# Kernel optimization log

Measured on AMD Instinct MI355X. Metric: run time of the kernel, lower is better.

Reference implementation:

```python
import jax, jax.numpy as jnp
import numpy as np

B, M, N, D, H = 8, 64, 64, 256, 8

def setup_inputs() -> dict:
    key = jax.random.key(0)
    kx, kq, kk, kv, ko = jax.random.split(key, 5)
    x = jax.random.normal(kx, (B, M, N, D), dtype=jnp.float32)
    q = jax.random.normal(kq, (H, D, D), dtype=jnp.float32)
    k = jax.random.normal(kk, (D, D), dtype=jnp.float32)
    v = jax.random.normal(kv, (D, D), dtype=jnp.float32)
    o = jax.random.normal(ko, (H, D, D), dtype=jnp.float32)
    return {"x": x, "q": q, "k": k, "v": v, "o": o}

def reference(x, q, k, v, o):
    # x: [b,m,n,d]; q,o: [h,d,d]; k,v: [d,d]
    Q = jnp.einsum('bmnd,hdk->bhmnk', x, q)      # [b,h,m,n,d]
    h_half = Q.shape[1] // 2
    Q1, Q2 = Q[:, :h_half], Q[:, h_half:]
    K = jnp.einsum('bmnd,dk->bmnk', x, k)        # [b,m,n,d]
    V = jnp.einsum('bmnd,dv->bmnv', x, v)        # [b,m,n,d]

    # Axis 1: attend along the m (row) axis for each column y
    logits1 = jnp.einsum('bhxyk,bzyk->bhyxz', Q1, K)   # [b,h/2,n,m,m]
    scores1 = jax.nn.softmax(logits1, axis=-1)
    O1 = jnp.einsum('bhyxz,bzyv->bhxyv', scores1, V)   # [b,h/2,m,n,d]

    # Axis 2: attend along the n (column) axis for each row x
    logits2 = jnp.einsum('bhxyk,bxzk->bhxyz', Q2, K)   # [b,h/2,m,n,n]
    scores2 = jax.nn.softmax(logits2, axis=-1)
    O2 = jnp.einsum('bhxyz,bxzv->bhxyv', scores2, V)   # [b,h/2,m,n,d]

    O = jnp.concatenate([O1, O2], axis=1)              # [b,h,m,n,d]
    # Faithful to original: 'bhmnd,hdv->bmnd' keeps d, sums over h and v
    Z = jnp.einsum('bhmnd,hdv->bmnd', O, o)
    return Z
```

## Files before the change

### kernel.cpp

```cpp
#include <hip/hip_runtime.h>

typedef unsigned short u16;
typedef __attribute__((ext_vector_type(8))) short short8;
typedef __attribute__((ext_vector_type(4))) float f32x4;

__device__ __forceinline__ float bf2f(u16 u){ return __uint_as_float(((unsigned)u)<<16); }
__device__ __forceinline__ u16 f2bf(float f){
  unsigned u = __float_as_uint(f);
  unsigned r = u + 0x7fffu + ((u>>16)&1u);
  return (u16)(r>>16);
}

#define MFMA16(a,b,c) __builtin_amdgcn_mfma_f32_16x16x32_bf16(a,b,c,0,0,0)

static constexpr int XS_STR  = 264;
static constexpr int PS_STR  = 72;
static constexpr int WT_STR  = 72;
static constexpr int XHI_OFF = 0;
static constexpr int XLO_OFF = 16896;
static constexpr int GT_OFF  = 33792;
static constexpr int XVT_OFF = 50688;
static constexpr int PS_OFF  = 69120;
static constexpr int SMEM_BYTES = 73728*2;

static constexpr int MH_SMEM = 70656*2;


__global__ void ksplit_kernel(const float* __restrict__ k,
                              u16* __restrict__ khi, u16* __restrict__ klo){
  int e = blockIdx.x*256 + threadIdx.x;
  float f = k[e];
  u16 hi = f2bf(f);
  khi[e] = hi;
  klo[e] = f2bf(f - bf2f(hi));
}

__global__ __launch_bounds__(256,1) void mh_kernel(
    const float* __restrict__ q, const u16* __restrict__ khi,
    const u16* __restrict__ klo, u16* __restrict__ mhi, u16* __restrict__ mlo)
{
  extern __shared__ u16 sm[];
  u16* Qhi = sm;
  u16* Qlo = sm + 16896;
  u16* Chi = sm + 33792;
  u16* Clo = sm + 52224;

  const int tid = threadIdx.x;
  const int w = tid >> 6, lane = tid & 63;
  const int quad = lane >> 4, m16 = lane & 15;
  const int cw = w << 6, koq = quad << 3;
  const int h = blockIdx.x >> 2, dt = (blockIdx.x & 3) << 6;

  #pragma unroll
  for (int i=0;i<16;i++){
    int idx4 = i*256 + tid;
    int tr = idx4 >> 6, c4 = (idx4 & 63) << 2;
    const float4 xv = *(const float4*)(q + (((h<<8)+dt+tr)<<8) + c4);
    ushort4 hv, lv;
    hv.x=f2bf(xv.x); lv.x=f2bf(xv.x-bf2f(hv.x));
    hv.y=f2bf(xv.y); lv.y=f2bf(xv.y-bf2f(hv.y));
    hv.z=f2bf(xv.z); lv.z=f2bf(xv.z-bf2f(hv.z));
    hv.w=f2bf(xv.w); lv.w=f2bf(xv.w-bf2f(hv.w));
    *(ushort4*)&Qhi[tr*XS_STR + c4] = hv;
    *(ushort4*)&Qlo[tr*XS_STR + c4] = lv;
  }
  __syncthreads();

  const f32x4 zf = {0.f,0.f,0.f,0.f};
  f32x4 acc[4][4];
  #pragma unroll
  for (int r=0;r<4;r++)
    #pragma unroll
    for (int c=0;c<4;c++) acc[r][c] = zf;

  short8 Bh[2][4], Bl[2][4];
  #pragma unroll
  for (int c=0;c<4;c++){
    Bh[0][c] = *(const short8*)&khi[(cw + c*16 + m16)*256 + koq];
    Bl[0][c] = *(const short8*)&klo[(cw + c*16 + m16)*256 + koq];
  }
  #pragma unroll
  for (int kk=0;kk<8;kk++){
    const int cur = kk&1, nxt = cur^1;
    if (kk<7){
      const int ko2 = ((kk+1)<<5) + koq;
      #pragma unroll
      for (int c=0;c<4;c++){
        Bh[nxt][c] = *(const short8*)&khi[(cw + c*16 + m16)*256 + ko2];
        Bl[nxt][c] = *(const short8*)&klo[(cw + c*16 + m16)*256 + ko2];
      }
    }
    const int ko = (kk<<5) + koq;
    short8 Ah[4], Al[4];
    #pragma unroll
    for (int r=0;r<4;r++) Ah[r] = *(const short8*)&Qhi[(r*16+m16)*XS_STR + ko];
    #pragma unroll
    for (int r=0;r<4;r++) Al[r] = *(const short8*)&Qlo[(r*16+m16)*XS_STR + ko];
    #pragma unroll
    for (int r=0;r<4;r++)
      #pragma unroll
      for (int c=0;c<4;c++){
        acc[r][c] = MFMA16(Ah[r], Bh[cur][c], acc[r][c]);
        acc[r][c] = MFMA16(Ah[r], Bl[cur][c], acc[r][c]);
        acc[r][c] = MFMA16(Al[r], Bh[cur][c], acc[r][c]);
      }
  }

  #pragma unroll
  for (int r=0;r<4;r++)
    #pragma unroll
    for (int c=0;c<4;c++)
      #pragma unroll
      for (int g=0; g<4; g++){
        int drow = r*16 + quad*4 + g;
        int dp   = cw + c*16 + m16;
        float vv = acc[r][c][g];
        u16 hh = f2bf(vv);
        Chi[dp*WT_STR + drow] = hh;
        Clo[dp*WT_STR + drow] = f2bf(vv - bf2f(hh));
      }
  __syncthreads();

  #pragma unroll
  for (int p=0;p<8;p++){
    int ch = tid + (p<<8);
    int dp = ch >> 3, i8 = (ch & 7) << 3;
    *(int4*)&mhi[(((h<<8)+dp)<<8) + dt + i8] = *(const int4*)&Chi[dp*WT_STR + i8];
    *(int4*)&mlo[(((h<<8)+dp)<<8) + dt + i8] = *(const int4*)&Clo[dp*WT_STR + i8];
  }
}

__global__ void vt_kernel(const float* __restrict__ v, u16* __restrict__ vT){
  __shared__ float Ts[64*65];
  const int tid = threadIdx.x;
  const int bi = (blockIdx.x>>2)<<6, bj = (blockIdx.x&3)<<6;
  #pragma unroll
  for (int p=0;p<4;p++){
    int idx4 = tid + (p<<8);
    int i = idx4 >> 4, c4 = (idx4 & 15) << 2;
    const float4 f4 = *(const float4*)(v + ((bi+i)<<8) + bj + c4);
    Ts[i*65+c4] = f4.x; Ts[i*65+c4+1] = f4.y; Ts[i*65+c4+2] = f4.z; Ts[i*65+c4+3] = f4.w;
  }
  __syncthreads();
  #pragma unroll
  for (int p=0;p<2;p++){
    int ch = tid + (p<<8);
    int j = ch >> 3, i8 = (ch & 7) << 3;
    short8 t8;
    #pragma unroll
    for (int e=0;e<8;e++) t8[e] = (short)f2bf(Ts[(i8+e)*65 + j]);
    *(short8*)&vT[((bj+j)<<8) + bi + i8] = t8;
  }
}

__global__ void so_kernel(const float* __restrict__ o, float* __restrict__ so){
  int h = blockIdx.x;
  int w = threadIdx.x >> 6, l = threadIdx.x & 63;
  for (int i=0;i<64;i++){
    int row = w*64 + i;
    const float4 f4 = *(const float4*)(o + (((h<<8)+row)<<8) + (l<<2));
    float s = f4.x + f4.y + f4.z + f4.w;
    #pragma unroll
    for (int off=32; off>=1; off>>=1) s += __shfl_xor(s, off, 64);
    if (l==0) so[(h<<8)+row] = s;
  }
}

template<int BR>
__global__ __launch_bounds__(256,1) void attn_kernel(
    const float* __restrict__ x, const u16* __restrict__ mhiP,
    const u16* __restrict__ mloP, const u16* __restrict__ vT,
    const float* __restrict__ soP, float* __restrict__ out)
{
  extern __shared__ u16 sm[];
  u16* Xhi = sm + XHI_OFF;
  u16* Xlo = sm + XLO_OFF;
  u16* Gt  = sm + GT_OFF;
  u16* Xvt = sm + XVT_OFF;
  u16* Ps  = sm + PS_OFF;

  const int tid  = threadIdx.x;
  const int w    = tid >> 6, lane = tid & 63;
  const int quad = lane >> 4, m16 = lane & 15;
  const int b    = blockIdx.x >> 6, s = blockIdx.x & 63;
  const int cw   = w << 6;
  const int koq  = quad << 3;

  auto tok = [&](int t)->int {
    int m = (BR==0) ? t : s;
    int n = (BR==0) ? s : t;
    return (((b<<6) + m) << 14) + (n << 8);
  };

  #pragma unroll
  for (int i=0;i<16;i++){
    int idx4 = i*256 + tid;
    int tr = idx4 >> 6, c4 = (idx4 & 63) << 2;
    const float4 xv = *(const float4*)(x + tok(tr) + c4);
    ushort4 hv, lv;
    hv.x=f2bf(xv.x); lv.x=f2bf(xv.x-bf2f(hv.x));
    hv.y=f2bf(xv.y); lv.y=f2bf(xv.y-bf2f(hv.y));
    hv.z=f2bf(xv.z); lv.z=f2bf(xv.z-bf2f(hv.z));
    hv.w=f2bf(xv.w); lv.w=f2bf(xv.w-bf2f(hv.w));
    *(ushort4*)&Xhi[tr*XS_STR + c4] = hv;
    *(ushort4*)&Xlo[tr*XS_STR + c4] = lv;
  }
  __syncthreads();

  const f32x4 zf = {0.f,0.f,0.f,0.f};
  f32x4 acc[4][4];

  auto mm3 = [&](const u16* __restrict__ Whi, const u16* __restrict__ Wlo){
    #pragma unroll
    for (int r=0;r<4;r++)
      #pragma unroll
      for (int c=0;c<4;c++) acc[r][c] = zf;
    short8 Bh[2][4], Bl[2][4];
    #pragma unroll
    for (int c=0;c<4;c++){
      Bh[0][c] = *(const short8*)&Whi[(cw + c*16 + m16)*256 + koq];
      Bl[0][c] = *(const short8*)&Wlo[(cw + c*16 + m16)*256 + koq];
    }
    #pragma unroll
    for (int kk=0;kk<8;kk++){
      const int cur = kk&1, nxt = cur^1;
      if (kk<7){
        const int ko2 = ((kk+1)<<5) + koq;
        #pragma unroll
        for (int c=0;c<4;c++){
          Bh[nxt][c] = *(const short8*)&Whi[(cw + c*16 + m16)*256 + ko2];
          Bl[nxt][c] = *(const short8*)&Wlo[(cw + c*16 + m16)*256 + ko2];
        }
      }
      const int ko = (kk<<5) + koq;
      short8 Ah[4], Al[4];
      #pragma unroll
      for (int r=0;r<4;r++) Ah[r] = *(const short8*)&Xhi[(r*16+m16)*XS_STR + ko];
      #pragma unroll
      for (int r=0;r<4;r++) Al[r] = *(const short8*)&Xlo[(r*16+m16)*XS_STR + ko];
      #pragma unroll
      for (int r=0;r<4;r++)
        #pragma unroll
        for (int c=0;c<4;c++){
          acc[r][c] = MFMA16(Ah[r], Bh[cur][c], acc[r][c]);
          acc[r][c] = MFMA16(Ah[r], Bl[cur][c], acc[r][c]);
          acc[r][c] = MFMA16(Al[r], Bh[cur][c], acc[r][c]);
        }
    }
  };

  {
    #pragma unroll
    for (int r=0;r<4;r++)
      #pragma unroll
      for (int c=0;c<4;c++) acc[r][c] = zf;
    #pragma unroll
    for (int kk=0;kk<8;kk++){
      const int ko = (kk<<5) + koq;
      short8 A[4], Bf[4];
      #pragma unroll
      for (int r=0;r<4;r++) A[r]  = *(const short8*)&Xhi[(r*16+m16)*XS_STR + ko];
      #pragma unroll
      for (int c=0;c<4;c++) Bf[c] = *(const short8*)&vT[(cw + c*16 + m16)*256 + ko];
      #pragma unroll
      for (int r=0;r<4;r++)
        #pragma unroll
        for (int c=0;c<4;c++) acc[r][c] = MFMA16(A[r], Bf[c], acc[r][c]);
    }
    #pragma unroll
    for (int r=0;r<4;r++)
      #pragma unroll
      for (int c=0;c<4;c++)
        #pragma unroll
        for (int g=0; g<4; g++){
          int z  = r*16 + quad*4 + g;
          int vc = cw + c*16 + m16;
          Xvt[vc*WT_STR + z] = f2bf(acc[r][c][g]);
        }
  }

  f32x4 Z[4][4];
  #pragma unroll
  for (int r=0;r<4;r++)
    #pragma unroll
    for (int c=0;c<4;c++) Z[r][c] = zf;

  for (int h=0; h<4; h++){
    const int gh = BR*4 + h;

    mm3(mhiP + gh*65536, mloP + gh*65536);
    #pragma unroll
    for (int r=0;r<4;r++)
      #pragma unroll
      for (int c=0;c<4;c++)
        #pragma unroll
        for (int g=0; g<4; g++){
          int row = r*16 + quad*4 + g;
          int col = cw + c*16 + m16;
          Gt[row*XS_STR + col] = f2bf(acc[r][c][g]);
        }
    __syncthreads();

    f32x4 L[4];
    #pragma unroll
    for (int c=0;c<4;c++) L[c] = zf;
    #pragma unroll
    for (int kk=0;kk<8;kk++){
      const int ko = (kk<<5) + koq;
      short8 A = *(const short8*)&Gt[(w*16+m16)*XS_STR + ko];
      #pragma unroll
      for (int c=0;c<4;c++)
        L[c] = MFMA16(A, *(const short8*)&Xhi[(c*16+m16)*XS_STR + ko], L[c]);
      #pragma unroll
      for (int c=0;c<4;c++)
        L[c] = MFMA16(A, *(const short8*)&Xlo[(c*16+m16)*XS_STR + ko], L[c]);
    }
    __syncthreads();
    #pragma unroll
    for (int r=0;r<4;r++)
      #pragma unroll
      for (int c=0;c<4;c++)
        #pragma unroll
        for (int g=0; g<4; g++){
          int row = r*16 + quad*4 + g;
          int col = cw + c*16 + m16;
          float vv = acc[r][c][g];
          u16 hh = f2bf(vv);
          Gt[row*XS_STR + col] = f2bf(vv - bf2f(hh));
        }
    __syncthreads();

    #pragma unroll
    for (int kk=0;kk<8;kk++){
      const int ko = (kk<<5) + koq;
      short8 A = *(const short8*)&Gt[(w*16+m16)*XS_STR + ko];
      #pragma unroll
      for (int c=0;c<4;c++)
        L[c] = MFMA16(A, *(const short8*)&Xhi[(c*16+m16)*XS_STR + ko], L[c]);
    }

    #pragma unroll
    for (int g=0; g<4; g++){
      float mx = fmaxf(fmaxf(L[0][g],L[1][g]), fmaxf(L[2][g],L[3][g]));
      #pragma unroll
      for (int off=1; off<16; off<<=1) mx = fmaxf(mx, __shfl_xor(mx, off, 64));
      float sum = 0.f;
      #pragma unroll
      for (int c=0;c<4;c++){ float e = __expf(L[c][g]-mx); L[c][g] = e; sum += e; }
      #pragma unroll
      for (int off=1; off<16; off<<=1) sum += __shfl_xor(sum, off, 64);
      float inv = 1.f / sum;
      int row = w*16 + quad*4 + g;
      #pragma unroll
      for (int c=0;c<4;c++) Ps[row*PS_STR + c*16 + m16] = f2bf(L[c][g]*inv);
    }
    __syncthreads();

    #pragma unroll
    for (int r=0;r<4;r++)
      #pragma unroll
      for (int c=0;c<4;c++) acc[r][c] = zf;
    #pragma unroll
    for (int kk=0;kk<2;kk++){
      const int ko = (kk<<5) + koq;
      short8 A[4], Bf[4];
      #pragma unroll
      for (int r=0;r<4;r++) A[r]  = *(const short8*)&Ps[(r*16+m16)*PS_STR + ko];
      #pragma unroll
      for (int c=0;c<4;c++) Bf[c] = *(const short8*)&Xvt[(cw + c*16 + m16)*WT_STR + ko];
      #pragma unroll
      for (int r=0;r<4;r++)
        #pragma unroll
        for (int c=0;c<4;c++) acc[r][c] = MFMA16(A[r], Bf[c], acc[r][c]);
    }
    float sc[4];
    #pragma unroll
    for (int c=0;c<4;c++) sc[c] = soP[gh*256 + cw + c*16 + m16];
    #pragma unroll
    for (int r=0;r<4;r++)
      #pragma unroll
      for (int c=0;c<4;c++)
        #pragma unroll
        for (int g=0; g<4; g++) Z[r][c][g] += sc[c]*acc[r][c][g];
  }

  #pragma unroll
  for (int r=0;r<4;r++)
    #pragma unroll
    for (int c=0;c<4;c++)
      #pragma unroll
      for (int g=0; g<4; g++){
        int t   = r*16 + quad*4 + g;
        int col = cw + c*16 + m16;
        int off = tok(t) + col;
        float vv = Z[r][c][g];
        if (BR==1) vv += out[off];
        out[off] = vv;
      }
}

extern "C" void kernel_launch(void* const* d_in, const int* in_sizes, int n_in,
                              void* d_out, int out_size, void* d_ws, size_t ws_size,
                              hipStream_t stream) {
  const float* x = (const float*)d_in[0];
  const float* q = (const float*)d_in[1];
  const float* k = (const float*)d_in[2];
  const float* v = (const float*)d_in[3];
  const float* o = (const float*)d_in[4];
  u16* ws   = (u16*)d_ws;
  u16* mhi  = ws;
  u16* mlo  = ws + 524288;
  u16* scr  = ws + 1048576;
  u16* khi  = scr;
  u16* klo  = scr + 65536;
  u16* vT   = scr;
  float* soP = (float*)(scr + 65536);
  float* out = (float*)d_out;

  ksplit_kernel<<<256, 256, 0, stream>>>(k, khi, klo);
  (void)hipFuncSetAttribute(reinterpret_cast<const void*>(&mh_kernel),
                            hipFuncAttributeMaxDynamicSharedMemorySize, MH_SMEM);
  mh_kernel<<<32, 256, MH_SMEM, stream>>>(q, khi, klo, mhi, mlo);
  vt_kernel<<<16, 256, 0, stream>>>(v, vT);
  so_kernel<<<8, 256, 0, stream>>>(o, soP);

  (void)hipFuncSetAttribute(reinterpret_cast<const void*>(&attn_kernel<0>),
                            hipFuncAttributeMaxDynamicSharedMemorySize, SMEM_BYTES);
  (void)hipFuncSetAttribute(reinterpret_cast<const void*>(&attn_kernel<1>),
                            hipFuncAttributeMaxDynamicSharedMemorySize, SMEM_BYTES);
  attn_kernel<0><<<512, 256, SMEM_BYTES, stream>>>(x, mhi, mlo, vT, soP, out);
  attn_kernel<1><<<512, 256, SMEM_BYTES, stream>>>(x, mhi, mlo, vT, soP, out);
}
```

Measured before the change: 404.0 us.

## Merge attention branches into one launch with 512-thread blocks and atomics

The two per-branch attention launches become a single 1024-block grid, and output is accumulated with atomicAdd into a zeroed buffer. Blocks grow to 512 threads (8 waves), each wave covering half the columns. The softmax row is split across two waves and recombined through a small shared-memory max/sum exchange. The k-split, v-transpose and o-rowsum prep kernels are fused into one wider launch. The aim is more waves per CU for latency hiding, lower per-thread register pressure and fewer launches. The cost is float atomics, an extra memset and an extra block-level barrier per head.

Result: faster. 355.1 us (-12.1%).

```diff
diff --git a/kernel.cpp b/kernel.cpp
--- a/kernel.cpp
+++ b/kernel.cpp
@@ -21,18 +21,62 @@
 static constexpr int GT_OFF  = 33792;
 static constexpr int XVT_OFF = 50688;
 static constexpr int PS_OFF  = 69120;
-static constexpr int SMEM_BYTES = 73728*2;
+static constexpr int SMRE_OFF= 73728;
+static constexpr int SMEM_BYTES = (73728 + 512)*2;
 
 static constexpr int MH_SMEM = 70656*2;
 
 
-__global__ void ksplit_kernel(const float* __restrict__ k,
-                              u16* __restrict__ khi, u16* __restrict__ klo){
-  int e = blockIdx.x*256 + threadIdx.x;
-  float f = k[e];
-  u16 hi = f2bf(f);
-  khi[e] = hi;
-  klo[e] = f2bf(f - bf2f(hi));
+__global__ void prep_kernel(const float* __restrict__ k, const float* __restrict__ v,
+                            const float* __restrict__ o, u16* __restrict__ khi,
+                            u16* __restrict__ klo, u16* __restrict__ vT,
+                            float* __restrict__ soP){
+  __shared__ float Ts[64*65];
+  const int blk = blockIdx.x, tid = threadIdx.x;
+  if (blk < 64){
+    int base = blk*1024 + tid*4;
+    const float4 f4 = *(const float4*)(k + base);
+    ushort4 hv, lv;
+    hv.x=f2bf(f4.x); lv.x=f2bf(f4.x-bf2f(hv.x));
+    hv.y=f2bf(f4.y); lv.y=f2bf(f4.y-bf2f(hv.y));
+    hv.z=f2bf(f4.z); lv.z=f2bf(f4.z-bf2f(hv.z));
+    hv.w=f2bf(f4.w); lv.w=f2bf(f4.w-bf2f(hv.w));
+    *(ushort4*)&khi[base] = hv;
+    *(ushort4*)&klo[base] = lv;
+  } else if (blk < 80){
+    int t = blk - 64;
+    const int bi = (t>>2)<<6, bj = (t&3)<<6;
+    #pragma unroll
+    for (int p=0;p<4;p++){
+      int idx4 = tid + (p<<8);
+      int i = idx4 >> 4, c4 = (idx4 & 15) << 2;
+      const float4 f4 = *(const float4*)(v + ((bi+i)<<8) + bj + c4);
+      Ts[i*65+c4]=f4.x; Ts[i*65+c4+1]=f4.y; Ts[i*65+c4+2]=f4.z; Ts[i*65+c4+3]=f4.w;
+    }
+    __syncthreads();
+    #pragma unroll
+    for (int p=0;p<2;p++){
+      int ch = tid + (p<<8);
+      int j = ch >> 3, i8 = (ch & 7) << 3;
+      short8 t8;
+      #pragma unroll
+      for (int e=0;e<8;e++) t8[e] = (short)f2bf(Ts[(i8+e)*65 + j]);
+      *(short8*)&vT[((bj+j)<<8) + bi + i8] = t8;
+    }
+  } else {
+    int p = blk - 80;
+    int h = p >> 5, base = (p & 31) << 3;
+    int w = tid >> 6, l = tid & 63;
+    #pragma unroll
+    for (int i=0;i<2;i++){
+      int row = base + w*2 + i;
+      const float4 f4 = *(const float4*)(o + (((h<<8)+row)<<8) + (l<<2));
+      float s = f4.x + f4.y + f4.z + f4.w;
+      #pragma unroll
+      for (int off=32; off>=1; off>>=1) s += __shfl_xor(s, off, 64);
+      if (l==0) soP[(h<<8)+row] = s;
+    }
+  }
 }
 
 __global__ __launch_bounds__(256,1) void mh_kernel(
@@ -130,44 +174,7 @@
   }
 }
 
-__global__ void vt_kernel(const float* __restrict__ v, u16* __restrict__ vT){
-  __shared__ float Ts[64*65];
-  const int tid = threadIdx.x;
-  const int bi = (blockIdx.x>>2)<<6, bj = (blockIdx.x&3)<<6;
-  #pragma unroll
-  for (int p=0;p<4;p++){
-    int idx4 = tid + (p<<8);
-    int i = idx4 >> 4, c4 = (idx4 & 15) << 2;
-    const float4 f4 = *(const float4*)(v + ((bi+i)<<8) + bj + c4);
-    Ts[i*65+c4] = f4.x; Ts[i*65+c4+1] = f4.y; Ts[i*65+c4+2] = f4.z; Ts[i*65+c4+3] = f4.w;
-  }
-  __syncthreads();
-  #pragma unroll
-  for (int p=0;p<2;p++){
-    int ch = tid + (p<<8);
-    int j = ch >> 3, i8 = (ch & 7) << 3;
-    short8 t8;
-    #pragma unroll
-    for (int e=0;e<8;e++) t8[e] = (short)f2bf(Ts[(i8+e)*65 + j]);
-    *(short8*)&vT[((bj+j)<<8) + bi + i8] = t8;
-  }
-}
-
-__global__ void so_kernel(const float* __restrict__ o, float* __restrict__ so){
-  int h = blockIdx.x;
-  int w = threadIdx.x >> 6, l = threadIdx.x & 63;
-  for (int i=0;i<64;i++){
-    int row = w*64 + i;
-    const float4 f4 = *(const float4*)(o + (((h<<8)+row)<<8) + (l<<2));
-    float s = f4.x + f4.y + f4.z + f4.w;
-    #pragma unroll
-    for (int off=32; off>=1; off>>=1) s += __shfl_xor(s, off, 64);
-    if (l==0) so[(h<<8)+row] = s;
-  }
-}
-
-template<int BR>
-__global__ __launch_bounds__(256,1) void attn_kernel(
+__global__ __launch_bounds__(512,2) void attn_kernel(
     const float* __restrict__ x, const u16* __restrict__ mhiP,
     const u16* __restrict__ mloP, const u16* __restrict__ vT,
     const float* __restrict__ soP, float* __restrict__ out)
@@ -178,23 +185,28 @@
   u16* Gt  = sm + GT_OFF;
   u16* Xvt = sm + XVT_OFF;
   u16* Ps  = sm + PS_OFF;
+  float* SMf = (float*)(sm + SMRE_OFF);
 
   const int tid  = threadIdx.x;
   const int w    = tid >> 6, lane = tid & 63;
   const int quad = lane >> 4, m16 = lane & 15;
-  const int b    = blockIdx.x >> 6, s = blockIdx.x & 63;
-  const int cw   = w << 6;
+  const int br   = blockIdx.x >> 9;
+  const int idx  = blockIdx.x & 511;
+  const int b    = idx >> 6, s = idx & 63;
+  const int cw   = w << 5;
+  const int rs   = (w >> 1) << 4;
+  const int zh   = w & 1;
   const int koq  = quad << 3;
 
   auto tok = [&](int t)->int {
-    int m = (BR==0) ? t : s;
-    int n = (BR==0) ? s : t;
+    int m = br ? s : t;
+    int n = br ? t : s;
     return (((b<<6) + m) << 14) + (n << 8);
   };
 
   #pragma unroll
-  for (int i=0;i<16;i++){
-    int idx4 = i*256 + tid;
+  for (int i=0;i<8;i++){
+    int idx4 = i*512 + tid;
     int tr = idx4 >> 6, c4 = (idx4 & 63) << 2;
     const float4 xv = *(const float4*)(x + tok(tr) + c4);
     ushort4 hv, lv;
@@ -208,16 +220,14 @@
   __syncthreads();
 
   const f32x4 zf = {0.f,0.f,0.f,0.f};
-  f32x4 acc[4][4];
+  f32x4 acc[4][2];
 
   auto mm3 = [&](const u16* __restrict__ Whi, const u16* __restrict__ Wlo){
     #pragma unroll
-    for (int r=0;r<4;r++)
-      #pragma unroll
-      for (int c=0;c<4;c++) acc[r][c] = zf;
-    short8 Bh[2][4], Bl[2][4];
-    #pragma unroll
-    for (int c=0;c<4;c++){
+    for (int r=0;r<4;r++){ acc[r][0] = zf; acc[r][1] = zf; }
+    short8 Bh[2][2], Bl[2][2];
+    #pragma unroll
+    for (int c=0;c<2;c++){
       Bh[0][c] = *(const short8*)&Whi[(cw + c*16 + m16)*256 + koq];
       Bl[0][c] = *(const short8*)&Wlo[(cw + c*16 + m16)*256 + koq];
     }
@@ -227,7 +237,7 @@
       if (kk<7){
         const int ko2 = ((kk+1)<<5) + koq;
         #pragma unroll
-        for (int c=0;c<4;c++){
+        for (int c=0;c<2;c++){
           Bh[nxt][c] = *(const short8*)&Whi[(cw + c*16 + m16)*256 + ko2];
           Bl[nxt][c] = *(const short8*)&Wlo[(cw + c*16 + m16)*256 + ko2];
         }
@@ -241,7 +251,7 @@
       #pragma unroll
       for (int r=0;r<4;r++)
         #pragma unroll
-        for (int c=0;c<4;c++){
+        for (int c=0;c<2;c++){
           acc[r][c] = MFMA16(Ah[r], Bh[cur][c], acc[r][c]);
           acc[r][c] = MFMA16(Ah[r], Bl[cur][c], acc[r][c]);
           acc[r][c] = MFMA16(Al[r], Bh[cur][c], acc[r][c]);
@@ -251,26 +261,24 @@
 
   {
     #pragma unroll
-    for (int r=0;r<4;r++)
-      #pragma unroll
-      for (int c=0;c<4;c++) acc[r][c] = zf;
+    for (int r=0;r<4;r++){ acc[r][0] = zf; acc[r][1] = zf; }
     #pragma unroll
     for (int kk=0;kk<8;kk++){
       const int ko = (kk<<5) + koq;
-      short8 A[4], Bf[4];
+      short8 A[4], Bf[2];
       #pragma unroll
       for (int r=0;r<4;r++) A[r]  = *(const short8*)&Xhi[(r*16+m16)*XS_STR + ko];
       #pragma unroll
-      for (int c=0;c<4;c++) Bf[c] = *(const short8*)&vT[(cw + c*16 + m16)*256 + ko];
+      for (int c=0;c<2;c++) Bf[c] = *(const short8*)&vT[(cw + c*16 + m16)*256 + ko];
       #pragma unroll
       for (int r=0;r<4;r++)
         #pragma unroll
-        for (int c=0;c<4;c++) acc[r][c] = MFMA16(A[r], Bf[c], acc[r][c]);
+        for (int c=0;c<2;c++) acc[r][c] = MFMA16(A[r], Bf[c], acc[r][c]);
     }
     #pragma unroll
     for (int r=0;r<4;r++)
       #pragma unroll
-      for (int c=0;c<4;c++)
+      for (int c=0;c<2;c++)
         #pragma unroll
         for (int g=0; g<4; g++){
           int z  = r*16 + quad*4 + g;
@@ -279,20 +287,18 @@
         }
   }
 
-  f32x4 Z[4][4];
-  #pragma unroll
-  for (int r=0;r<4;r++)
-    #pragma unroll
-    for (int c=0;c<4;c++) Z[r][c] = zf;
+  f32x4 Z[4][2];
+  #pragma unroll
+  for (int r=0;r<4;r++){ Z[r][0] = zf; Z[r][1] = zf; }
 
   for (int h=0; h<4; h++){
-    const int gh = BR*4 + h;
+    const int gh = br*4 + h;
 
     mm3(mhiP + gh*65536, mloP + gh*65536);
     #pragma unroll
     for (int r=0;r<4;r++)
       #pragma unroll
-      for (int c=0;c<4;c++)
+      for (int c=0;c<2;c++)
         #pragma unroll
         for (int g=0; g<4; g++){
           int row = r*16 + quad*4 + g;
@@ -301,25 +307,24 @@
         }
     __syncthreads();
 
-    f32x4 L[4];
-    #pragma unroll
-    for (int c=0;c<4;c++) L[c] = zf;
+    f32x4 L[2];
+    L[0] = zf; L[1] = zf;
     #pragma unroll
     for (int kk=0;kk<8;kk++){
       const int ko = (kk<<5) + koq;
-      short8 A = *(const short8*)&Gt[(w*16+m16)*XS_STR + ko];
-      #pragma unroll
-      for (int c=0;c<4;c++)
-        L[c] = MFMA16(A, *(const short8*)&Xhi[(c*16+m16)*XS_STR + ko], L[c]);
-      #pragma unroll
-      for (int c=0;c<4;c++)
-        L[c] = MFMA16(A, *(const short8*)&Xlo[(c*16+m16)*XS_STR + ko], L[c]);
+      short8 A = *(const short8*)&Gt[(rs+m16)*XS_STR + ko];
+      #pragma unroll
+      for (int c=0;c<2;c++)
+        L[c] = MFMA16(A, *(const short8*)&Xhi[((zh<<5) + c*16+m16)*XS_STR + ko], L[c]);
+      #pragma unroll
+      for (int c=0;c<2;c++)
+        L[c] = MFMA16(A, *(const short8*)&Xlo[((zh<<5) + c*16+m16)*XS_STR + ko], L[c]);
     }
     __syncthreads();
     #pragma unroll
     for (int r=0;r<4;r++)
       #pragma unroll
-      for (int c=0;c<4;c++)
+      for (int c=0;c<2;c++)
         #pragma unroll
         for (int g=0; g<4; g++){
           int row = r*16 + quad*4 + g;
@@ -333,53 +338,67 @@
     #pragma unroll
     for (int kk=0;kk<8;kk++){
       const int ko = (kk<<5) + koq;
-      short8 A = *(const short8*)&Gt[(w*16+m16)*XS_STR + ko];
-      #pragma unroll
-      for (int c=0;c<4;c++)
-        L[c] = MFMA16(A, *(const short8*)&Xhi[(c*16+m16)*XS_STR + ko], L[c]);
-    }
-
+      short8 A = *(const short8*)&Gt[(rs+m16)*XS_STR + ko];
+      #pragma unroll
+      for (int c=0;c<2;c++)
+        L[c] = MFMA16(A, *(const short8*)&Xhi[((zh<<5) + c*16+m16)*XS_STR + ko], L[c]);
+    }
+
+    float mxl[4], sml[4];
     #pragma unroll
     for (int g=0; g<4; g++){
-      float mx = fmaxf(fmaxf(L[0][g],L[1][g]), fmaxf(L[2][g],L[3][g]));
+      float mx = fmaxf(L[0][g], L[1][g]);
       #pragma unroll
       for (int off=1; off<16; off<<=1) mx = fmaxf(mx, __shfl_xor(mx, off, 64));
       float sum = 0.f;
       #pragma unroll
-      for (int c=0;c<4;c++){ float e = __expf(L[c][g]-mx); L[c][g] = e; sum += e; }
+      for (int c=0;c<2;c++){ float e = __expf(L[c][g]-mx); L[c][g] = e; sum += e; }
       #pragma unroll
       for (int off=1; off<16; off<<=1) sum += __shfl_xor(sum, off, 64);
-      float inv = 1.f / sum;
-      int row = w*16 + quad*4 + g;
-      #pragma unroll
-      for (int c=0;c<4;c++) Ps[row*PS_STR + c*16 + m16] = f2bf(L[c][g]*inv);
-    }
-    __syncthreads();
-
-    #pragma unroll
-    for (int r=0;r<4;r++)
-      #pragma unroll
-      for (int c=0;c<4;c++) acc[r][c] = zf;
+      mxl[g] = mx; sml[g] = sum;
+      if (m16 == 0){
+        int row = rs + quad*4 + g;
+        SMf[row*4 + zh*2]     = mx;
+        SMf[row*4 + zh*2 + 1] = sum;
+      }
+    }
+    __syncthreads();
+    #pragma unroll
+    for (int g=0; g<4; g++){
+      int row = rs + quad*4 + g;
+      float mxo = SMf[row*4 + (zh^1)*2];
+      float smo = SMf[row*4 + (zh^1)*2 + 1];
+      float M   = fmaxf(mxl[g], mxo);
+      float al  = __expf(mxl[g]-M), ao = __expf(mxo-M);
+      float scale = al / (sml[g]*al + smo*ao);
+      #pragma unroll
+      for (int c=0;c<2;c++)
+        Ps[row*PS_STR + (zh<<5) + c*16 + m16] = f2bf(L[c][g]*scale);
+    }
+    __syncthreads();
+
+    #pragma unroll
+    for (int r=0;r<4;r++){ acc[r][0] = zf; acc[r][1] = zf; }
     #pragma unroll
     for (int kk=0;kk<2;kk++){
       const int ko = (kk<<5) + koq;
-      short8 A[4], Bf[4];
+      short8 A[4], Bf[2];
       #pragma unroll
       for (int r=0;r<4;r++) A[r]  = *(const short8*)&Ps[(r*16+m16)*PS_STR + ko];
       #pragma unroll
-      for (int c=0;c<4;c++) Bf[c] = *(const short8*)&Xvt[(cw + c*16 + m16)*WT_STR + ko];
+      for (int c=0;c<2;c++) Bf[c] = *(const short8*)&Xvt[(cw + c*16 + m16)*WT_STR + ko];
       #pragma unroll
       for (int r=0;r<4;r++)
         #pragma unroll
-        for (int c=0;c<4;c++) acc[r][c] = MFMA16(A[r], Bf[c], acc[r][c]);
-    }
-    float sc[4];
-    #pragma unroll
-    for (int c=0;c<4;c++) sc[c] = soP[gh*256 + cw + c*16 + m16];
+        for (int c=0;c<2;c++) acc[r][c] = MFMA16(A[r], Bf[c], acc[r][c]);
+    }
+    float sc[2];
+    sc[0] = soP[gh*256 + cw + m16];
+    sc[1] = soP[gh*256 + cw + 16 + m16];
     #pragma unroll
     for (int r=0;r<4;r++)
       #pragma unroll
-      for (int c=0;c<4;c++)
+      for (int c=0;c<2;c++)
         #pragma unroll
         for (int g=0; g<4; g++) Z[r][c][g] += sc[c]*acc[r][c][g];
   }
@@ -387,15 +406,12 @@
   #pragma unroll
   for (int r=0;r<4;r++)
     #pragma unroll
-    for (int c=0;c<4;c++)
+    for (int c=0;c<2;c++)
       #pragma unroll
       for (int g=0; g<4; g++){
         int t   = r*16 + quad*4 + g;
         int col = cw + c*16 + m16;
-        int off = tok(t) + col;
-        float vv = Z[r][c][g];
-        if (BR==1) vv += out[off];
-        out[off] = vv;
+        atomicAdd(&out[tok(t) + col], Z[r][c][g]);
       }
 }
 
@@ -410,24 +426,19 @@
   u16* ws   = (u16*)d_ws;
   u16* mhi  = ws;
   u16* mlo  = ws + 524288;
-  u16* scr  = ws + 1048576;
-  u16* khi  = scr;
-  u16* klo  = scr + 65536;
-  u16* vT   = scr;
-  float* soP = (float*)(scr + 65536);
+  u16* khi  = ws + 1048576;
+  u16* klo  = ws + 1114112;
+  u16* vT   = ws + 1179648;
+  float* soP = (float*)(ws + 1245184);
   float* out = (float*)d_out;
 
-  ksplit_kernel<<<256, 256, 0, stream>>>(k, khi, klo);
+  (void)hipMemsetAsync(d_out, 0, (size_t)out_size*sizeof(float), stream);
+  prep_kernel<<<336, 256, 0, stream>>>(k, v, o, khi, klo, vT, soP);
   (void)hipFuncSetAttribute(reinterpret_cast<const void*>(&mh_kernel),
                             hipFuncAttributeMaxDynamicSharedMemorySize, MH_SMEM);
   mh_kernel<<<32, 256, MH_SMEM, stream>>>(q, khi, klo, mhi, mlo);
-  vt_kernel<<<16, 256, 0, stream>>>(v, vT);
-  so_kernel<<<8, 256, 0, stream>>>(o, soP);
-
-  (void)hipFuncSetAttribute(reinterpret_cast<const void*>(&attn_kernel<0>),
+
+  (void)hipFuncSetAttribute(reinterpret_cast<const void*>(&attn_kernel),
                             hipFuncAttributeMaxDynamicSharedMemorySize, SMEM_BYTES);
-  (void)hipFuncSetAttribute(reinterpret_cast<const void*>(&attn_kernel<1>),
-                            hipFuncAttributeMaxDynamicSharedMemorySize, SMEM_BYTES);
-  attn_kernel<0><<<512, 256, SMEM_BYTES, stream>>>(x, mhi, mlo, vT, soP, out);
-  attn_kernel<1><<<512, 256, SMEM_BYTES, stream>>>(x, mhi, mlo, vT, soP, out);
+  attn_kernel<<<1024, 512, SMEM_BYTES, stream>>>(x, mhi, mlo, vT, soP, out);
 }
```
